# Optimization experiments

Hardware: AMD Instinct MI355X
Metric: run time of the kernel (lower is better)

Reference implementation:

```python
import jax, jax.numpy as jnp
import numpy as np
from jax import lax

VOCAB = 32000
EMB = 512
HID = 1024
BATCH = 64
MAX_LEN = 30
STEPS = MAX_LEN + 2
SOS = 1
PAD = 0


def setup_inputs() -> dict:
    key = jax.random.key(0)
    ks = jax.random.split(key, 9)
    s = 0.05
    target = jax.random.randint(ks[0], (BATCH, 1), 0, VOCAB)
    encoder_hidden = jax.random.normal(ks[1], (1, BATCH, HID), dtype=jnp.float32)
    emb = jax.random.normal(ks[2], (VOCAB, EMB), dtype=jnp.float32) * s
    emb = emb.at[PAD].set(0.0)  # padding_idx row zeroed like torch
    W_ih = jax.random.normal(ks[3], (3 * HID, EMB), dtype=jnp.float32) * s
    W_hh = jax.random.normal(ks[4], (3 * HID, HID), dtype=jnp.float32) * s
    b_ih = jax.random.normal(ks[5], (3 * HID,), dtype=jnp.float32) * s
    b_hh = jax.random.normal(ks[6], (3 * HID,), dtype=jnp.float32) * s
    fc_W = jax.random.normal(ks[7], (VOCAB, HID), dtype=jnp.float32) * s
    fc_b = jax.random.normal(ks[8], (VOCAB,), dtype=jnp.float32) * s
    return {"target": target, "encoder_hidden": encoder_hidden, "emb": emb,
            "W_ih": W_ih, "W_hh": W_hh, "b_ih": b_ih, "b_hh": b_hh,
            "fc_W": fc_W, "fc_b": fc_b}


def reference(target, encoder_hidden, emb, W_ih, W_hh, b_ih, b_hh, fc_W, fc_b):
    B = target.shape[0]

    def step(carry, _):
        tok, h = carry                      # tok [B] int, h [B,H]
        x = emb[tok]                        # [B,E] embedding lookup
        gi = x @ W_ih.T + b_ih              # [B,3H]
        gh = h @ W_hh.T + b_hh              # [B,3H]
        i_r, i_z, i_n = jnp.split(gi, 3, axis=-1)
        h_r, h_z, h_n = jnp.split(gh, 3, axis=-1)
        r = jax.nn.sigmoid(i_r + h_r)
        z = jax.nn.sigmoid(i_z + h_z)
        n = jnp.tanh(i_n + r * h_n)
        h_new = (1.0 - z) * n + z * h       # torch GRU update
        logits = h_new @ fc_W.T + fc_b      # [B,V]
        logp = jax.nn.log_softmax(logits, axis=-1)
        tok_new = jnp.argmax(logp, axis=-1)  # greedy feedback (topk, k=1)
        return (tok_new, h_new), logp

    h0 = encoder_hidden[0]                  # num_layers == 1
    tok0 = jnp.full((B,), SOS, dtype=jnp.int32)
    (_, hT), outs = lax.scan(step, (tok0, h0), None, length=STEPS)
    decoder_outputs = jnp.transpose(outs, (1, 0, 2))  # [B, STEPS, V]
    return decoder_outputs, hT[None]
```

## Files before the change

kernel.cpp:

```cpp
#include <hip/hip_runtime.h>

#define VV 32000
#define EE 512
#define HH 1024
#define NB 64
#define NSTEP 32

typedef __attribute__((ext_vector_type(8))) short short8;
typedef __attribute__((ext_vector_type(4))) float f32x4;
typedef unsigned long long u64;

#define MFMA16(a, b, c) __builtin_amdgcn_mfma_f32_16x16x32_bf16((a), (b), (c), 0, 0, 0)

__device__ __forceinline__ unsigned short f2bf(float f) {
  unsigned int u = __float_as_uint(f);
  u += 0x7fffu + ((u >> 16) & 1u);
  return (unsigned short)(u >> 16);
}
__device__ __forceinline__ float bf2f(unsigned short b) {
  return __uint_as_float(((unsigned int)b) << 16);
}
__device__ __forceinline__ float sigmoidf_(float x) { return 1.0f / (1.0f + expf(-x)); }
__device__ __forceinline__ unsigned int ordkey(float f) {
  unsigned int u = __float_as_uint(f);
  return u ^ ((u >> 31) ? 0xFFFFFFFFu : 0x80000000u);
}
__device__ __forceinline__ float ordkey_inv(unsigned int u) {
  return __uint_as_float((u & 0x80000000u) ? (u ^ 0x80000000u) : ~u);
}

__global__ __launch_bounds__(256) void prep_wcat(const float* __restrict__ Wih,
                                                 const float* __restrict__ Whh,
                                                 unsigned short* __restrict__ wm,
                                                 unsigned short* __restrict__ wr) {
  int ub = blockIdx.x / 3, g = blockIdx.x % 3;
  for (int e = threadIdx.x; e < 48 * 512; e += 256) {
    int ks = e >> 9, lane = (e >> 3) & 63, j = e & 7;
    int row = g * HH + ub * 16 + (lane & 15);
    int k = ks * 32 + ((lane >> 4) << 3) + j;
    float f = (k < EE) ? Wih[(size_t)row * EE + k] : Whh[(size_t)row * HH + (k - EE)];
    unsigned short m_ = f2bf(f);
    size_t idx = (((size_t)(ub * 3 + g) * 48 + ks) * 64 + lane) * 8 + j;
    wm[idx] = m_;
    wr[idx] = f2bf(f - bf2f(m_));
  }
}

__global__ __launch_bounds__(256) void prep_wfc(const float* __restrict__ fcW,
                                                unsigned short* __restrict__ wfc) {
  int vg = blockIdx.x;
  for (int e = threadIdx.x; e < 32768; e += 256) {
    int ks = e >> 10, n = (e >> 9) & 1, lane = (e >> 3) & 63, j = e & 7;
    int v = vg * 32 + n * 16 + (lane & 15);
    int k = ks * 32 + ((lane >> 4) << 3) + j;
    wfc[(((size_t)vg * 32 + ks) * 2 + n) * 512 + lane * 8 + j] = f2bf(fcW[(size_t)v * HH + k]);
  }
}

__global__ __launch_bounds__(256) void init_kernel(
    const float* __restrict__ enc, const float* __restrict__ emb, float* __restrict__ h4a,
    unsigned short* __restrict__ ham, unsigned short* __restrict__ har,
    unsigned short* __restrict__ xam, unsigned short* __restrict__ xar,
    int* __restrict__ cnt) {
  int i = blockIdx.x * 256 + threadIdx.x;
  int b = i >> 10, u = i & 1023;
  float hv = enc[i];
  h4a[i] = hv;
  unsigned short m_ = f2bf(hv);
  size_t idx = (((size_t)(b >> 4) * 32 + (u >> 5)) * 64 + ((b & 15) + (((u >> 3) & 3) << 4))) * 8 + (u & 7);
  ham[idx] = m_;
  har[idx] = f2bf(hv - bf2f(m_));
  if (i < NB * EE) {
    int b2 = i >> 9, k = i & 511;
    float xv = emb[EE + k];
    unsigned short xm = f2bf(xv);
    size_t xi = (((size_t)(b2 >> 4) * 16 + (k >> 5)) * 64 + ((b2 & 15) + (((k >> 3) & 3) << 4))) * 8 + (k & 7);
    xam[xi] = xm;
    xar[xi] = f2bf(xv - bf2f(xm));
  }
  if (i < NB) cnt[i] = 0;
}


__device__ __forceinline__ void gru_body(
    int bid, int tid, float (*red)[16][65],
    const unsigned short* xam, const unsigned short* xar,
    const unsigned short* him, const unsigned short* hir,
    const float* h4in, float* h4out,
    const unsigned short* wm, const unsigned short* wrs,
    const float* bih, const float* bhh,
    unsigned short* hom, unsigned short* hor) {
  const int lane = tid & 63, w = tid >> 6;
  const int ub = bid >> 2, mg = bid & 3;
  f32x4 aR{}, aZ{}, aNX{}, aNH{};
  const short8* XM = (const short8*)xam;
  const short8* XR = (const short8*)xar;
  const short8* HM = (const short8*)him;
  const short8* HR = (const short8*)hir;
  const short8* WM = (const short8*)wm;
  const short8* WR = (const short8*)wrs;
#pragma unroll
  for (int s = 0; s < 12; ++s) {
    int ks = w * 12 + s;
    short8 am, ar;
    if (ks < 16) {
      int o = (mg * 16 + ks) * 64 + lane;
      am = XM[o]; ar = XR[o];
    } else {
      int o = (mg * 32 + (ks - 16)) * 64 + lane;
      am = HM[o]; ar = HR[o];
    }
    {
      int o = ((ub * 3 + 0) * 48 + ks) * 64 + lane;
      short8 wmv = WM[o], wrv = WR[o];
      aR = MFMA16(am, wmv, aR); aR = MFMA16(ar, wmv, aR); aR = MFMA16(am, wrv, aR);
    }
    {
      int o = ((ub * 3 + 1) * 48 + ks) * 64 + lane;
      short8 wmv = WM[o], wrv = WR[o];
      aZ = MFMA16(am, wmv, aZ); aZ = MFMA16(ar, wmv, aZ); aZ = MFMA16(am, wrv, aZ);
    }
    {
      int o = ((ub * 3 + 2) * 48 + ks) * 64 + lane;
      short8 wmv = WM[o], wrv = WR[o];
      if (ks < 16) {
        aNX = MFMA16(am, wmv, aNX); aNX = MFMA16(ar, wmv, aNX); aNX = MFMA16(am, wrv, aNX);
      } else {
        aNH = MFMA16(am, wmv, aNH); aNH = MFMA16(ar, wmv, aNH); aNH = MFMA16(am, wrv, aNH);
      }
    }
  }
#pragma unroll
  for (int reg = 0; reg < 4; ++reg) {
    int rr = ((lane >> 4) << 2) + reg, c = lane & 15;
    red[w][rr][c] = aR[reg];
    red[w][rr][16 + c] = aZ[reg];
    red[w][rr][32 + c] = aNX[reg];
    red[w][rr][48 + c] = aNH[reg];
  }
  __syncthreads();
  const int mrow = tid >> 4, uu = tid & 15;
  float R = 0.f, Z = 0.f, NX = 0.f, NH = 0.f;
#pragma unroll
  for (int q = 0; q < 4; ++q) {
    R += red[q][mrow][uu];
    Z += red[q][mrow][16 + uu];
    NX += red[q][mrow][32 + uu];
    NH += red[q][mrow][48 + uu];
  }
  const int b = mg * 16 + mrow, u = ub * 16 + uu;
  float r = sigmoidf_(R + bih[u] + bhh[u]);
  float z = sigmoidf_(Z + bih[HH + u] + bhh[HH + u]);
  float n = tanhf(NX + bih[2 * HH + u] + r * (NH + bhh[2 * HH + u]));
  float hold = h4in[b * HH + u];
  float hn = (1.0f - z) * n + z * hold;
  h4out[b * HH + u] = hn;
  unsigned short m_ = f2bf(hn);
  size_t idx = (((size_t)(b >> 4) * 32 + (u >> 5)) * 64 + ((b & 15) + (((u >> 3) & 3) << 4))) * 8 + (u & 7);
  hom[idx] = m_;
  hor[idx] = f2bf(hn - bf2f(m_));
}

__device__ __forceinline__ void fc_body(
    int bid, int tid, float (*red)[64][33],
    const unsigned short* ham,
    const unsigned short* wfc, const float* fcb,
    float* out, u64* blkkeys, int t) {
  const int lane = tid & 63, w = tid >> 6;
  const int vg = bid;
  f32x4 acc[4][2] = {};
  const short8* HM = (const short8*)ham;
  const short8* W = (const short8*)wfc;
#pragma unroll
  for (int s = 0; s < 8; ++s) {
    int ks = w * 8 + s;
    short8 am[4], wv[2];
#pragma unroll
    for (int m = 0; m < 4; ++m) am[m] = HM[(m * 32 + ks) * 64 + lane];
#pragma unroll
    for (int nt = 0; nt < 2; ++nt) wv[nt] = W[((vg * 32 + ks) * 2 + nt) * 64 + lane];
#pragma unroll
    for (int m = 0; m < 4; ++m)
#pragma unroll
      for (int nt = 0; nt < 2; ++nt)
        acc[m][nt] = MFMA16(am[m], wv[nt], acc[m][nt]);
  }
#pragma unroll
  for (int m = 0; m < 4; ++m)
#pragma unroll
    for (int nt = 0; nt < 2; ++nt)
#pragma unroll
      for (int reg = 0; reg < 4; ++reg)
        red[w][m * 16 + ((lane >> 4) << 2) + reg][nt * 16 + (lane & 15)] = acc[m][nt][reg];
  __syncthreads();
  const int b = tid >> 2, c0 = (tid & 3) << 3;
  u64 k1 = 0;
  size_t ro = ((size_t)b * NSTEP + t) * VV + (size_t)vg * 32 + c0;
#pragma unroll
  for (int e = 0; e < 8; ++e) {
    int c = c0 + e;
    float v = red[0][b][c] + red[1][b][c] + red[2][b][c] + red[3][b][c] + fcb[vg * 32 + c];
    out[ro + e] = v;
    u64 key = ((u64)ordkey(v) << 32) | (u64)(0xFFFFFFFFu - (unsigned)(vg * 32 + c));
    if (key > k1) k1 = key;
  }
  {
    u64 o1 = __shfl_xor(k1, 1, 64);
    if (o1 > k1) k1 = o1;
    u64 o2 = __shfl_xor(k1, 2, 64);
    if (o2 > k1) k1 = o2;
  }
  if ((tid & 3) == 0) blkkeys[(size_t)b * 1000 + vg] = k1;
}

__global__ __launch_bounds__(256, 4) void gru_kernel(
    const unsigned short* xam, const unsigned short* xar,
    const unsigned short* him, const unsigned short* hir,
    const float* h4in, float* h4out,
    const unsigned short* wm, const unsigned short* wrs,
    const float* bih, const float* bhh,
    unsigned short* hom, unsigned short* hor) {
  __shared__ float red[4][16][65];
  gru_body(blockIdx.x, threadIdx.x, red, xam, xar, him, hir, h4in, h4out, wm, wrs, bih, bhh, hom, hor);
}

__global__ __launch_bounds__(256, 4) void fc_kernel(
    const unsigned short* ham,
    const unsigned short* wfc, const float* fcb,
    float* out, u64* blkkeys, int t) {
  __shared__ float red[4][64][33];
  fc_body(blockIdx.x, threadIdx.x, red, ham, wfc, fcb, out, blkkeys, t);
}

__global__ __launch_bounds__(256) void sel1_kernel(
    const float* __restrict__ out, const u64* __restrict__ blkkeys,
    int* __restrict__ cnt, int* __restrict__ cand, int t) {
  const int b = blockIdx.x >> 3, q = blockIdx.x & 7;
  const int tid = threadIdx.x;
  __shared__ u64 skey[256];
  const u64* kb = blkkeys + (size_t)b * 1000;
  u64 mk = 0;
  for (int i = tid; i < 1000; i += 256) {
    u64 k = kb[i];
    if (k > mk) mk = k;
  }
  skey[tid] = mk;
  __syncthreads();
  for (int off = 128; off > 0; off >>= 1) {
    if (tid < off && skey[tid + off] > skey[tid]) skey[tid] = skey[tid + off];
    __syncthreads();
  }
  const float Mf = ordkey_inv((unsigned)(skey[0] >> 32));
  const float thr = Mf - 0.10f;
  const float* rowp = out + ((size_t)b * NSTEP + t) * VV;
  for (int v = q * (VV / 8) + tid; v < (q + 1) * (VV / 8); v += 256) {
    if (rowp[v] >= thr) {
      int p = atomicAdd(&cnt[b], 1);
      if (p < 256) cand[b * 256 + p] = v;
    }
  }
}

__global__ __launch_bounds__(256) void sel2_kernel(
    int* __restrict__ cnt, const int* __restrict__ cand,
    const float* __restrict__ fcW, const float* __restrict__ fcb,
    const float* __restrict__ emb, const float* __restrict__ h4,
    unsigned short* __restrict__ xam, unsigned short* __restrict__ xar) {
  const int b = blockIdx.x, tid = threadIdx.x;
  __shared__ int scand[256];
  __shared__ u64 rkey[256];
  __shared__ int stok;
  int n = cnt[b];
  if (n > 256) n = 256;
  for (int i = tid; i < n; i += 256) scand[i] = cand[b * 256 + i];
  __syncthreads();
  const int w = tid >> 6, ln = tid & 63;
  for (int ci = w; ci < n; ci += 4) {
    int v = scand[ci];
    float p = 0.f;
#pragma unroll
    for (int q = 0; q < 16; ++q)
      p += h4[b * HH + ln + (q << 6)] * fcW[(size_t)v * HH + ln + (q << 6)];
#pragma unroll
    for (int d = 1; d < 64; d <<= 1) p += __shfl_xor(p, d);
    if (ln == 0)
      rkey[ci] = ((u64)ordkey(p + fcb[v]) << 32) | (u64)(0xFFFFFFFFu - (unsigned)v);
  }
  __syncthreads();
  if (tid == 0) {
    u64 bk = 0;
    for (int ci = 0; ci < n; ++ci)
      if (rkey[ci] > bk) bk = rkey[ci];
    stok = (int)(0xFFFFFFFFu - (unsigned)(bk & 0xFFFFFFFFu));
    cnt[b] = 0;
  }
  __syncthreads();
  const int tok = stok;
  for (int k = tid; k < EE; k += 256) {
    float xv = emb[(size_t)tok * EE + k];
    unsigned short xm = f2bf(xv);
    size_t xi = (((size_t)(b >> 4) * 16 + (k >> 5)) * 64 + ((b & 15) + (((k >> 3) & 3) << 4))) * 8 + (k & 7);
    xam[xi] = xm;
    xar[xi] = f2bf(xv - bf2f(xm));
  }
}

__global__ __launch_bounds__(256) void lsm_kernel(float* __restrict__ out) {
  const int bt = blockIdx.x;
  const int tid = threadIdx.x;
  float* row = out + (size_t)bt * VV;
  float4* r4 = (float4*)row;
  __shared__ float mred[256], sred[256];
  float m = -INFINITY, s = 0.f;
  for (int i = tid; i < VV / 4; i += 256) {
    float4 v = r4[i];
#pragma unroll
    for (int c = 0; c < 4; ++c) {
      float x = (&v.x)[c];
      if (x > m) { s = s * expf(m - x) + 1.0f; m = x; }
      else s += expf(x - m);
    }
  }
  mred[tid] = m; sred[tid] = s;
  __syncthreads();
  for (int off = 128; off > 0; off >>= 1) {
    if (tid < off) {
      float m1 = mred[tid], s1 = sred[tid];
      float m2 = mred[tid + off], s2 = sred[tid + off];
      float M = fmaxf(m1, m2);
      mred[tid] = M;
      sred[tid] = s1 * expf(m1 - M) + s2 * expf(m2 - M);
    }
    __syncthreads();
  }
  const float lse = mred[0] + logf(sred[0]);
  for (int i = tid; i < VV / 4; i += 256) {
    float4 v = r4[i];
    v.x -= lse; v.y -= lse; v.z -= lse; v.w -= lse;
    r4[i] = v;
  }
}

__global__ __launch_bounds__(256) void final_kernel(const float* __restrict__ h4,
                                                    float* __restrict__ out) {
  int i = blockIdx.x * 256 + threadIdx.x;
  out[(size_t)NB * NSTEP * VV + i] = h4[i];
}

extern "C" void kernel_launch(void* const* d_in, const int* in_sizes, int n_in,
                              void* d_out, int out_size, void* d_ws, size_t ws_size,
                              hipStream_t stream) {
  const float* enc = (const float*)d_in[1];
  const float* emb = (const float*)d_in[2];
  const float* Wih = (const float*)d_in[3];
  const float* Whh = (const float*)d_in[4];
  const float* bih = (const float*)d_in[5];
  const float* bhh = (const float*)d_in[6];
  const float* fcW = (const float*)d_in[7];
  const float* fcb = (const float*)d_in[8];
  float* out = (float*)d_out;

  char* ws = (char*)d_ws;
  unsigned short* wfc = (unsigned short*)ws; ws += (size_t)32768000 * 2;
  unsigned short* wcm = (unsigned short*)ws; ws += (size_t)4718592 * 2;
  unsigned short* wcr = (unsigned short*)ws; ws += (size_t)4718592 * 2;
  unsigned short* hAm = (unsigned short*)ws; ws += (size_t)65536 * 2;
  unsigned short* hAr = (unsigned short*)ws; ws += (size_t)65536 * 2;
  unsigned short* hBm = (unsigned short*)ws; ws += (size_t)65536 * 2;
  unsigned short* hBr = (unsigned short*)ws; ws += (size_t)65536 * 2;
  unsigned short* xam = (unsigned short*)ws; ws += (size_t)32768 * 2;
  unsigned short* xar = (unsigned short*)ws; ws += (size_t)32768 * 2;
  float* h4a = (float*)ws; ws += (size_t)NB * HH * 4;
  float* h4b = (float*)ws; ws += (size_t)NB * HH * 4;
  u64* blkkeys = (u64*)ws; ws += (size_t)NB * 1000 * 8;
  int* cnt = (int*)ws; ws += (size_t)NB * 4;
  int* cand = (int*)ws; ws += (size_t)NB * 256 * 4;

  prep_wfc<<<1000, 256, 0, stream>>>(fcW, wfc);
  prep_wcat<<<192, 256, 0, stream>>>(Wih, Whh, wcm, wcr);
  init_kernel<<<256, 256, 0, stream>>>(enc, emb, h4a, hAm, hAr, xam, xar, cnt);

  for (int t = 0; t < NSTEP; ++t) {
    const float* hin = (t & 1) ? h4b : h4a;
    float* hout = (t & 1) ? h4a : h4b;
    const unsigned short* him = (t & 1) ? hBm : hAm;
    const unsigned short* hir = (t & 1) ? hBr : hAr;
    unsigned short* hom = (t & 1) ? hAm : hBm;
    unsigned short* hor = (t & 1) ? hAr : hBr;
    gru_kernel<<<256, 256, 0, stream>>>(xam, xar, him, hir, hin, hout, wcm, wcr, bih, bhh, hom, hor);
    fc_kernel<<<1000, 256, 0, stream>>>(hom, wfc, fcb, out, blkkeys, t);
    sel1_kernel<<<512, 256, 0, stream>>>(out, blkkeys, cnt, cand, t);
    sel2_kernel<<<64, 256, 0, stream>>>(cnt, cand, fcW, fcb, emb, hout, xam, xar);
  }
  lsm_kernel<<<2048, 256, 0, stream>>>(out);
  final_kernel<<<256, 256, 0, stream>>>(h4a, out);
}
```

Before: 1.932 ms.

## Split FC GEMM by batch rows per wave, removing LDS reduction

The FC logits kernel used to split the K dimension across 4 waves and then reduce the partial sums through shared memory with a barrier. Now each wave owns 16 batch rows and loops over the full K=1024, so the result is complete in registers. Bias add, output store and argmax key reduction happen directly from the accumulators, using lane shuffles. This removes the LDS traffic and the sync, and raises occupancy to 8 blocks per SM. The cost is that every wave loads the same weight tile, a 4x redundant read of fc_W per block, though the cache may absorb it, and each wave's serial MFMA chain is now longer.

```diff
diff --git a/kernel.cpp b/kernel.cpp
--- a/kernel.cpp
+++ b/kernel.cpp
@@ -81,7 +81,6 @@
   if (i < NB) cnt[i] = 0;
 }
 
-
 __device__ __forceinline__ void gru_body(
     int bid, int tid, float (*red)[16][65],
     const unsigned short* xam, const unsigned short* xar,
@@ -161,58 +160,6 @@
   hor[idx] = f2bf(hn - bf2f(m_));
 }
 
-__device__ __forceinline__ void fc_body(
-    int bid, int tid, float (*red)[64][33],
-    const unsigned short* ham,
-    const unsigned short* wfc, const float* fcb,
-    float* out, u64* blkkeys, int t) {
-  const int lane = tid & 63, w = tid >> 6;
-  const int vg = bid;
-  f32x4 acc[4][2] = {};
-  const short8* HM = (const short8*)ham;
-  const short8* W = (const short8*)wfc;
-#pragma unroll
-  for (int s = 0; s < 8; ++s) {
-    int ks = w * 8 + s;
-    short8 am[4], wv[2];
-#pragma unroll
-    for (int m = 0; m < 4; ++m) am[m] = HM[(m * 32 + ks) * 64 + lane];
-#pragma unroll
-    for (int nt = 0; nt < 2; ++nt) wv[nt] = W[((vg * 32 + ks) * 2 + nt) * 64 + lane];
-#pragma unroll
-    for (int m = 0; m < 4; ++m)
-#pragma unroll
-      for (int nt = 0; nt < 2; ++nt)
-        acc[m][nt] = MFMA16(am[m], wv[nt], acc[m][nt]);
-  }
-#pragma unroll
-  for (int m = 0; m < 4; ++m)
-#pragma unroll
-    for (int nt = 0; nt < 2; ++nt)
-#pragma unroll
-      for (int reg = 0; reg < 4; ++reg)
-        red[w][m * 16 + ((lane >> 4) << 2) + reg][nt * 16 + (lane & 15)] = acc[m][nt][reg];
-  __syncthreads();
-  const int b = tid >> 2, c0 = (tid & 3) << 3;
-  u64 k1 = 0;
-  size_t ro = ((size_t)b * NSTEP + t) * VV + (size_t)vg * 32 + c0;
-#pragma unroll
-  for (int e = 0; e < 8; ++e) {
-    int c = c0 + e;
-    float v = red[0][b][c] + red[1][b][c] + red[2][b][c] + red[3][b][c] + fcb[vg * 32 + c];
-    out[ro + e] = v;
-    u64 key = ((u64)ordkey(v) << 32) | (u64)(0xFFFFFFFFu - (unsigned)(vg * 32 + c));
-    if (key > k1) k1 = key;
-  }
-  {
-    u64 o1 = __shfl_xor(k1, 1, 64);
-    if (o1 > k1) k1 = o1;
-    u64 o2 = __shfl_xor(k1, 2, 64);
-    if (o2 > k1) k1 = o2;
-  }
-  if ((tid & 3) == 0) blkkeys[(size_t)b * 1000 + vg] = k1;
-}
-
 __global__ __launch_bounds__(256, 4) void gru_kernel(
     const unsigned short* xam, const unsigned short* xar,
     const unsigned short* him, const unsigned short* hir,
@@ -224,12 +171,52 @@
   gru_body(blockIdx.x, threadIdx.x, red, xam, xar, him, hir, h4in, h4out, wm, wrs, bih, bhh, hom, hor);
 }
 
-__global__ __launch_bounds__(256, 4) void fc_kernel(
-    const unsigned short* ham,
-    const unsigned short* wfc, const float* fcb,
-    float* out, u64* blkkeys, int t) {
-  __shared__ float red[4][64][33];
-  fc_body(blockIdx.x, threadIdx.x, red, ham, wfc, fcb, out, blkkeys, t);
+__global__ __launch_bounds__(256, 8) void fc_kernel(
+    const unsigned short* __restrict__ ham,
+    const unsigned short* __restrict__ wfc, const float* __restrict__ fcb,
+    float* __restrict__ out, u64* __restrict__ blkkeys, int t) {
+  const int tid = threadIdx.x;
+  const int lane = tid & 63, w = tid >> 6;
+  const int vg = blockIdx.x;
+  f32x4 acc0{}, acc1{};
+  const short8* HM = (const short8*)ham + (size_t)w * 2048;
+  const short8* W = (const short8*)wfc + (size_t)vg * 4096;
+#pragma unroll 8
+  for (int ks = 0; ks < 32; ++ks) {
+    short8 am = HM[ks * 64 + lane];
+    short8 w0 = W[(ks * 2 + 0) * 64 + lane];
+    short8 w1 = W[(ks * 2 + 1) * 64 + lane];
+    acc0 = MFMA16(am, w0, acc0);
+    acc1 = MFMA16(am, w1, acc1);
+  }
+  const int r0 = lane >> 4, c0 = lane & 15;
+  const float b0 = fcb[vg * 32 + c0];
+  const float b1 = fcb[vg * 32 + 16 + c0];
+  u64 kk[4];
+#pragma unroll
+  for (int reg = 0; reg < 4; ++reg) {
+    const int b = w * 16 + r0 * 4 + reg;
+    float v0 = acc0[reg] + b0;
+    float v1 = acc1[reg] + b1;
+    size_t ro = ((size_t)b * NSTEP + t) * VV + (size_t)vg * 32 + c0;
+    out[ro] = v0;
+    out[ro + 16] = v1;
+    u64 k0 = ((u64)ordkey(v0) << 32) | (u64)(0xFFFFFFFFu - (unsigned)(vg * 32 + c0));
+    u64 k1 = ((u64)ordkey(v1) << 32) | (u64)(0xFFFFFFFFu - (unsigned)(vg * 32 + 16 + c0));
+    kk[reg] = k0 > k1 ? k0 : k1;
+  }
+#pragma unroll
+  for (int d = 1; d < 16; d <<= 1)
+#pragma unroll
+    for (int reg = 0; reg < 4; ++reg) {
+      u64 o = __shfl_xor(kk[reg], d, 64);
+      if (o > kk[reg]) kk[reg] = o;
+    }
+  if (c0 == 0) {
+#pragma unroll
+    for (int reg = 0; reg < 4; ++reg)
+      blkkeys[(size_t)(w * 16 + r0 * 4 + reg) * 1000 + vg] = kk[reg];
+  }
 }
 
 __global__ __launch_bounds__(256) void sel1_kernel(
```

New measurement: 1.829 ms. 1.06x faster.
